# Optimization experiments

Hardware: AMD Instinct MI355X
Metric: run time of the kernel (lower is better)

The kernel has to match this reference:

```python
import jax, jax.numpy as jnp
import numpy as np

B, H, I = 131072, 128, 128  # batch, hidden_size, input_size (must be equal per source math)


def setup_inputs() -> dict:
    key = jax.random.key(0)
    ks = jax.random.split(key, 7)
    return {
        "x":   jax.random.normal(ks[0], (B, H), dtype=jnp.float32),
        "h_0": jax.random.normal(ks[1], (B, H), dtype=jnp.float32),
        "c_0": jax.random.normal(ks[2], (B, H), dtype=jnp.float32),
        "ih":  jax.random.normal(ks[3], (4 * H, I), dtype=jnp.float32) * 0.1,
        "hh":  jax.random.normal(ks[4], (4 * H, H), dtype=jnp.float32) * 0.1,
        "ib":  jax.random.normal(ks[5], (4 * H,), dtype=jnp.float32) * 0.1,
        "hb":  jax.random.normal(ks[6], (4 * H,), dtype=jnp.float32) * 0.1,
    }


def reference(x, h_0, c_0, ih, hh, ib, hb):
    hidden = hh.shape[1]
    # torch.split(ih, H) -> 4 chunks [H, I]; gate = x @ chunk (note: NOT chunk.T)
    ih4 = ih.reshape(4, hidden, -1)        # [4, H, I]
    hh4 = hh.reshape(4, hidden, hidden)    # [4, H, H]
    ib4 = ib.reshape(4, 1, hidden)
    hb4 = hb.reshape(4, 1, hidden)
    # combined gate GEMM: gates[g] = x @ ih4[g] + ib4[g] + h_0 @ hh4[g] + hb4[g]
    gates = (jnp.einsum('bh,ghi->gbi', x, ih4)
             + jnp.einsum('bh,ghk->gbk', h_0, hh4)
             + ib4 + hb4)                  # [4, B, H]
    I_g, F_g, G_g, O_g = gates[0], gates[1], gates[2], gates[3]
    c_1 = c_0 * jax.nn.sigmoid(F_g) + jax.nn.sigmoid(I_g) * jnp.tanh(G_g)
    h_1 = jax.nn.sigmoid(O_g) + jnp.tanh(c_1)  # faithful to source (additive, not gated)
    return (h_1, c_1, I_g, F_g, G_g, O_g)
```

## Files before the change

kernel.cpp:

```cpp
#include <hip/hip_runtime.h>
#include <hip/hip_bf16.h>

typedef __attribute__((ext_vector_type(8))) short short8;
typedef __attribute__((ext_vector_type(4))) float f32x4;

#define HSZ 128
#define BM  32
#define NT  512

__device__ __forceinline__ unsigned short f2bf(float f) {
    union { float f; unsigned int u; } c; c.f = f;
    return (unsigned short)((c.u + 0x7FFFu + ((c.u >> 16) & 1u)) >> 16);
}

__global__ void prep_kernel(const float* __restrict__ ih, const float* __restrict__ hh,
                            const float* __restrict__ ib, const float* __restrict__ hb,
                            unsigned short* __restrict__ Wp, float* __restrict__ bias) {
    int tid = blockIdx.x * blockDim.x + threadIdx.x;
    int col = tid >> 5;
    int kg  = tid & 31;
    int g = col >> 7, i = col & 127;
    short8 pk;
    #pragma unroll
    for (int j = 0; j < 8; ++j) {
        int k = kg * 8 + j;
        float v = (k < HSZ) ? ih[(g * HSZ + k) * HSZ + i]
                            : hh[(g * HSZ + (k - HSZ)) * HSZ + i];
        pk[j] = (short)f2bf(v);
    }
    *reinterpret_cast<short8*>(Wp + col * 256 + kg * 8) = pk;
    if (kg == 0) bias[col] = ib[col] + hb[col];
}

__global__ __launch_bounds__(NT, 6)
void lstm_kernel(const float* __restrict__ x, const float* __restrict__ h0,
                 const float* __restrict__ c0,
                 const unsigned short* __restrict__ Wp,
                 const float* __restrict__ biasp,
                 float* __restrict__ out, long BH) {
    constexpr int PITCH = 264;
    __shared__ unsigned short A_lds[BM * PITCH];
    __shared__ float S[8][640];

    const int t = threadIdx.x;
    const long rowBase = (long)blockIdx.x * BM;

    {
        const float4* x4 = reinterpret_cast<const float4*>(x + rowBase * HSZ);
        const float4* h4 = reinterpret_cast<const float4*>(h0 + rowBase * HSZ);
        #pragma unroll
        for (int j = 0; j < 2; ++j) {
            int fi = t + j * NT;
            int row = fi >> 5;
            int c4  = fi & 31;
            float4 vx = x4[fi];
            float4 vh = h4[fi];
            ushort4 px; px.x = f2bf(vx.x); px.y = f2bf(vx.y); px.z = f2bf(vx.z); px.w = f2bf(vx.w);
            ushort4 ph; ph.x = f2bf(vh.x); ph.y = f2bf(vh.y); ph.z = f2bf(vh.z); ph.w = f2bf(vh.w);
            *reinterpret_cast<ushort4*>(&A_lds[row * PITCH + c4 * 4]) = px;
            *reinterpret_cast<ushort4*>(&A_lds[row * PITCH + HSZ + c4 * 4]) = ph;
        }
    }
    __syncthreads();

    const int lane = t & 63;
    const int wid  = t >> 6;
    const int wn = wid;
    const int lr = lane & 15;
    const int lk = lane >> 4;

    const char* Ab = reinterpret_cast<const char*>(A_lds) + lr * (PITCH * 2) + lk * 16;
    const char* Wb = reinterpret_cast<const char*>(Wp) + (wn * 16 + lr) * 512 + lk * 16;

    f32x4 acc[2][4] = {};

    #pragma unroll
    for (int ks = 0; ks < 8; ++ks) {
        short8 a0 = *reinterpret_cast<const short8*>(Ab + ks * 64);
        short8 a1 = *reinterpret_cast<const short8*>(Ab + 16 * (PITCH * 2) + ks * 64);
        #pragma unroll
        for (int g = 0; g < 4; ++g) {
            short8 w = *reinterpret_cast<const short8*>(Wb + (g * 128) * 512 + ks * 64);
            acc[0][g] = __builtin_amdgcn_mfma_f32_16x16x32_bf16(w, a0, acc[0][g], 0, 0, 0);
            acc[1][g] = __builtin_amdgcn_mfma_f32_16x16x32_bf16(w, a1, acc[1][g], 0, 0, 0);
        }
    }

    f32x4 c0v[2];
    #pragma unroll
    for (int mi = 0; mi < 2; ++mi) {
        long pos = (rowBase + mi * 16 + lr) * HSZ + wn * 16 + lk * 4;
        c0v[mi] = *reinterpret_cast<const f32x4*>(c0 + pos);
    }

    #pragma unroll
    for (int g = 0; g < 4; ++g) {
        f32x4 bg = *reinterpret_cast<const f32x4*>(biasp + g * HSZ + wn * 16 + lk * 4);
        acc[0][g] += bg;
        acc[1][g] += bg;
    }

    float* slot = S[wid];
    const int rr0 = lane >> 2;
    const int gg0 = lane & 3;
    const long cb = (long)(wn * 16 + gg0 * 4);

    f32x4 c1v[2], h1v[2];
    #pragma unroll
    for (int mi = 0; mi < 2; ++mi) {
        #pragma unroll
        for (int r = 0; r < 4; ++r) {
            float iv = acc[mi][0][r];
            float fv = acc[mi][1][r];
            float gv = acc[mi][2][r];
            float ov = acc[mi][3][r];
            float si = 1.f / (1.f + __expf(-iv));
            float sf = 1.f / (1.f + __expf(-fv));
            float tg = 1.f - 2.f / (__expf(2.f * gv) + 1.f);
            float so = 1.f / (1.f + __expf(-ov));
            float c1 = c0v[mi][r] * sf + si * tg;
            float th = 1.f - 2.f / (__expf(2.f * c1) + 1.f);
            c1v[mi][r] = c1;
            h1v[mi][r] = so + th;
        }
    }

    #define PUT(V) do { \
        *reinterpret_cast<f32x4*>(&slot[(0 * 16 + lr) * 20 + lk * 4]) = (V)[0]; \
        *reinterpret_cast<f32x4*>(&slot[(16 + lr) * 20 + lk * 4])     = (V)[1]; \
    } while (0)
    #define FLS(OB) do { \
        f32x4 v0 = *reinterpret_cast<const f32x4*>(&slot[rr0 * 20 + gg0 * 4]); \
        f32x4 v1 = *reinterpret_cast<const f32x4*>(&slot[(16 + rr0) * 20 + gg0 * 4]); \
        __builtin_nontemporal_store(v0, reinterpret_cast<f32x4*>(out + (OB) + (rowBase + rr0) * HSZ + cb)); \
        __builtin_nontemporal_store(v1, reinterpret_cast<f32x4*>(out + (OB) + (rowBase + 16 + rr0) * HSZ + cb)); \
    } while (0)

    PUT(c1v);  FLS(BH);
    PUT(h1v);  FLS(0);
    { f32x4 p[2] = { acc[0][0], acc[1][0] }; PUT(p); FLS(2 * BH); }
    { f32x4 p[2] = { acc[0][1], acc[1][1] }; PUT(p); FLS(3 * BH); }
    { f32x4 p[2] = { acc[0][2], acc[1][2] }; PUT(p); FLS(4 * BH); }
    { f32x4 p[2] = { acc[0][3], acc[1][3] }; PUT(p); FLS(5 * BH); }
    #undef PUT
    #undef FLS
}

extern "C" void kernel_launch(void* const* d_in, const int* in_sizes, int n_in,
                              void* d_out, int out_size, void* d_ws, size_t ws_size,
                              hipStream_t stream) {
    const float* x  = (const float*)d_in[0];
    const float* h0 = (const float*)d_in[1];
    const float* c0 = (const float*)d_in[2];
    const float* ih = (const float*)d_in[3];
    const float* hh = (const float*)d_in[4];
    const float* ib = (const float*)d_in[5];
    const float* hb = (const float*)d_in[6];
    float* out = (float*)d_out;

    unsigned short* Wp = (unsigned short*)d_ws;
    float* bias = (float*)((char*)d_ws + 512 * 256 * 2);

    long BH = in_sizes[2];
    long B  = BH / HSZ;

    prep_kernel<<<64, 256, 0, stream>>>(ih, hh, ib, hb, Wp, bias);
    lstm_kernel<<<(int)(B / BM), NT, 0, stream>>>(x, h0, c0, Wp, bias, out, BH);
}
```

Before: 213.9 us.

## Stage epilogue through block-wide swizzled LDS tile for full-row coalesced stores

Replaces the per-wave 16x20 staging slots with a block-wide 32x128 fp32 tile, double-buffered and aliased with the bf16 A operand through a union. Each output is written to LDS with an XOR swizzle, then stored so every thread writes contiguous 16-byte chunks that cover full 512-byte rows. The aim is to turn partial-row global stores into fully coalesced row writes and to reduce LDS footprint for occupancy. The cost is six extra block-level barriers and a c1 round-trip through LDS.

```diff
diff --git a/kernel.cpp b/kernel.cpp
--- a/kernel.cpp
+++ b/kernel.cpp
@@ -32,6 +32,11 @@
     if (kg == 0) bias[col] = ib[col] + hb[col];
 }
 
+union SMem {
+    unsigned short A[BM * 264];
+    f32x4 T[2][BM * 32];
+};
+
 __global__ __launch_bounds__(NT, 6)
 void lstm_kernel(const float* __restrict__ x, const float* __restrict__ h0,
                  const float* __restrict__ c0,
@@ -39,8 +44,7 @@
                  const float* __restrict__ biasp,
                  float* __restrict__ out, long BH) {
     constexpr int PITCH = 264;
-    __shared__ unsigned short A_lds[BM * PITCH];
-    __shared__ float S[8][640];
+    __shared__ SMem sm;
 
     const int t = threadIdx.x;
     const long rowBase = (long)blockIdx.x * BM;
@@ -57,8 +61,8 @@
             float4 vh = h4[fi];
             ushort4 px; px.x = f2bf(vx.x); px.y = f2bf(vx.y); px.z = f2bf(vx.z); px.w = f2bf(vx.w);
             ushort4 ph; ph.x = f2bf(vh.x); ph.y = f2bf(vh.y); ph.z = f2bf(vh.z); ph.w = f2bf(vh.w);
-            *reinterpret_cast<ushort4*>(&A_lds[row * PITCH + c4 * 4]) = px;
-            *reinterpret_cast<ushort4*>(&A_lds[row * PITCH + HSZ + c4 * 4]) = ph;
+            *reinterpret_cast<ushort4*>(&sm.A[row * PITCH + c4 * 4]) = px;
+            *reinterpret_cast<ushort4*>(&sm.A[row * PITCH + HSZ + c4 * 4]) = ph;
         }
     }
     __syncthreads();
@@ -69,7 +73,7 @@
     const int lr = lane & 15;
     const int lk = lane >> 4;
 
-    const char* Ab = reinterpret_cast<const char*>(A_lds) + lr * (PITCH * 2) + lk * 16;
+    const char* Ab = reinterpret_cast<const char*>(sm.A) + lr * (PITCH * 2) + lk * 16;
     const char* Wb = reinterpret_cast<const char*>(Wp) + (wn * 16 + lr) * 512 + lk * 16;
 
     f32x4 acc[2][4] = {};
@@ -100,50 +104,76 @@
         acc[1][g] += bg;
     }
 
-    float* slot = S[wid];
-    const int rr0 = lane >> 2;
-    const int gg0 = lane & 3;
-    const long cb = (long)(wn * 16 + gg0 * 4);
+    __syncthreads();
 
-    f32x4 c1v[2], h1v[2];
+    #define SIDX(MI) ((MI * 16 + lr) * 32 + ((wn * 4 + lk) ^ (lr & 7)))
+
+    auto flush = [&](const f32x4* T, long obase) {
+        #pragma unroll
+        for (int p = 0; p < 2; ++p) {
+            int f = t + p * NT;
+            int row = f >> 5, c = f & 31;
+            f32x4 v = T[row * 32 + (c ^ (row & 7))];
+            __builtin_nontemporal_store(v,
+                reinterpret_cast<f32x4*>(out + obase + (rowBase + row) * (long)HSZ + c * 4));
+        }
+    };
+
     #pragma unroll
     for (int mi = 0; mi < 2; ++mi) {
+        f32x4 v;
         #pragma unroll
         for (int r = 0; r < 4; ++r) {
             float iv = acc[mi][0][r];
             float fv = acc[mi][1][r];
             float gv = acc[mi][2][r];
-            float ov = acc[mi][3][r];
             float si = 1.f / (1.f + __expf(-iv));
             float sf = 1.f / (1.f + __expf(-fv));
             float tg = 1.f - 2.f / (__expf(2.f * gv) + 1.f);
+            v[r] = c0v[mi][r] * sf + si * tg;
+        }
+        sm.T[0][SIDX(mi)] = v;
+    }
+    __syncthreads();
+
+    flush(sm.T[0], BH);
+    #pragma unroll
+    for (int mi = 0; mi < 2; ++mi) {
+        f32x4 c1 = sm.T[0][SIDX(mi)];
+        f32x4 v;
+        #pragma unroll
+        for (int r = 0; r < 4; ++r) {
+            float ov = acc[mi][3][r];
             float so = 1.f / (1.f + __expf(-ov));
-            float c1 = c0v[mi][r] * sf + si * tg;
-            float th = 1.f - 2.f / (__expf(2.f * c1) + 1.f);
-            c1v[mi][r] = c1;
-            h1v[mi][r] = so + th;
+            float th = 1.f - 2.f / (__expf(2.f * c1[r]) + 1.f);
+            v[r] = so + th;
         }
+        sm.T[1][SIDX(mi)] = v;
     }
+    __syncthreads();
 
-    #define PUT(V) do { \
-        *reinterpret_cast<f32x4*>(&slot[(0 * 16 + lr) * 20 + lk * 4]) = (V)[0]; \
-        *reinterpret_cast<f32x4*>(&slot[(16 + lr) * 20 + lk * 4])     = (V)[1]; \
-    } while (0)
-    #define FLS(OB) do { \
-        f32x4 v0 = *reinterpret_cast<const f32x4*>(&slot[rr0 * 20 + gg0 * 4]); \
-        f32x4 v1 = *reinterpret_cast<const f32x4*>(&slot[(16 + rr0) * 20 + gg0 * 4]); \
-        __builtin_nontemporal_store(v0, reinterpret_cast<f32x4*>(out + (OB) + (rowBase + rr0) * HSZ + cb)); \
-        __builtin_nontemporal_store(v1, reinterpret_cast<f32x4*>(out + (OB) + (rowBase + 16 + rr0) * HSZ + cb)); \
-    } while (0)
+    flush(sm.T[1], 0);
+    #pragma unroll
+    for (int mi = 0; mi < 2; ++mi) sm.T[0][SIDX(mi)] = acc[mi][0];
+    __syncthreads();
 
-    PUT(c1v);  FLS(BH);
-    PUT(h1v);  FLS(0);
-    { f32x4 p[2] = { acc[0][0], acc[1][0] }; PUT(p); FLS(2 * BH); }
-    { f32x4 p[2] = { acc[0][1], acc[1][1] }; PUT(p); FLS(3 * BH); }
-    { f32x4 p[2] = { acc[0][2], acc[1][2] }; PUT(p); FLS(4 * BH); }
-    { f32x4 p[2] = { acc[0][3], acc[1][3] }; PUT(p); FLS(5 * BH); }
-    #undef PUT
-    #undef FLS
+    flush(sm.T[0], 2 * BH);
+    #pragma unroll
+    for (int mi = 0; mi < 2; ++mi) sm.T[1][SIDX(mi)] = acc[mi][1];
+    __syncthreads();
+
+    flush(sm.T[1], 3 * BH);
+    #pragma unroll
+    for (int mi = 0; mi < 2; ++mi) sm.T[0][SIDX(mi)] = acc[mi][2];
+    __syncthreads();
+
+    flush(sm.T[0], 4 * BH);
+    #pragma unroll
+    for (int mi = 0; mi < 2; ++mi) sm.T[1][SIDX(mi)] = acc[mi][3];
+    __syncthreads();
+
+    flush(sm.T[1], 5 * BH);
+    #undef SIDX
 }
 
 extern "C" void kernel_launch(void* const* d_in, const int* in_sizes, int n_in,
```

New measurement: 197.6 us. 7.6% less time.
